# Performance work log

Hardware: AMD Instinct MI355X
Metric: run time of the kernel (lower is better)

Reference implementation:

```python
import jax, jax.numpy as jnp
import numpy as np

B, T, F, H, O = 16384, 128, 9, 128, 12


def setup_inputs() -> dict:
    key = jax.random.key(0)
    ks = jax.random.split(key, 14)
    s = 1.0 / np.sqrt(H)
    u = lambda k, shp: jax.random.uniform(k, shp, jnp.float32, -s, s)
    return {
        "x": jax.random.normal(ks[0], (B, T, F), jnp.float32),
        "W_in": u(ks[1], (H, F)), "b_in": u(ks[2], (H,)),
        "Wih0": u(ks[3], (4 * H, H)), "Whh0": u(ks[4], (4 * H, H)),
        "bih0": u(ks[5], (4 * H,)), "bhh0": u(ks[6], (4 * H,)),
        "Wih1": u(ks[7], (4 * H, H)), "Whh1": u(ks[8], (4 * H, H)),
        "bih1": u(ks[9], (4 * H,)), "bhh1": u(ks[10], (4 * H,)),
        "W_out": u(ks[11], (O, H)), "b_out": u(ks[12], (O,)),
    }


def _cell(h, c, xp, Wih, Whh, bih, bhh):
    # PyTorch LSTM gate order: i, f, g, o
    g = xp @ Wih.T + bih + h @ Whh.T + bhh  # [B, 4H]
    i, f, gg, o = jnp.split(g, 4, axis=-1)
    c = jax.nn.sigmoid(f) * c + jax.nn.sigmoid(i) * jnp.tanh(gg)
    h = jax.nn.sigmoid(o) * jnp.tanh(c)
    return h, c


def reference(x, W_in, b_in, Wih0, Whh0, bih0, bhh0, Wih1, Whh1, bih1, bhh1, W_out, b_out):
    # input projection, all timesteps at once: [B, T, H] -> scan over time
    xp = jnp.einsum('btf,hf->tbh', x, W_in) + b_in
    b = x.shape[0]
    zeros = jnp.zeros((b, H), x.dtype)
    carry0 = (zeros, zeros, zeros, zeros)  # h0, c0, h1, c1

    def step(carry, xt):
        h0, c0, h1, c1 = carry
        h0, c0 = _cell(h0, c0, xt, Wih0, Whh0, bih0, bhh0)
        h1, c1 = _cell(h1, c1, h0, Wih1, Whh1, bih1, bhh1)
        return (h0, c0, h1, c1), None

    (h0, c0, h1, c1), _ = jax.lax.scan(step, carry0, xp)
    # torch forward returns only the LAST step's output: out(h1) with softmax over dim=1
    return jax.nn.softmax(h1 @ W_out.T + b_out, axis=1)
```

## Files before the change

kernel.cpp:

```cpp
#include <hip/hip_runtime.h>
#include <stdint.h>
#include <stddef.h>

#define T_STEPS 128
#define F_IN 9
#define HID 128
#define OUT_N 12
#define XROW (T_STEPS * F_IN)

typedef __attribute__((ext_vector_type(8))) short bf16x8;
typedef __attribute__((ext_vector_type(4))) float f32x4;

#define MFMA16(a, b, c) __builtin_amdgcn_mfma_f32_16x16x32_bf16((a), (b), (c), 0, 0, 0)

__device__ __forceinline__ short f2bf(float f) {
  union { float f; uint32_t u; } v; v.f = f;
  return (short)((v.u + 0x7fffu + ((v.u >> 16) & 1u)) >> 16);
}
__device__ __forceinline__ float frcp(float x) { return __builtin_amdgcn_rcpf(x); }
__device__ __forceinline__ float fexp2(float x) { return __builtin_amdgcn_exp2f(x); }
__device__ __forceinline__ float tanh_f(float x) {
  return 1.0f - 2.0f * frcp(1.0f + fexp2(2.8853900817779268f * x));
}

__global__ void prep_w0x(const float* __restrict__ W_in, const float* __restrict__ b_in,
                         const float* __restrict__ Wih0, const float* __restrict__ bih0,
                         const float* __restrict__ bhh0, const float* __restrict__ bih1,
                         const float* __restrict__ bhh1,
                         short* __restrict__ w0xf, float* __restrict__ b0x, float* __restrict__ b1) {
  int tid = threadIdx.x;
  int nt = tid >> 4, hl = tid & 15;
  int w = nt >> 2, g = nt & 3;
  int n = g * 128 + w * 16 + hl;
  float wacc[F_IN];
#pragma unroll
  for (int f = 0; f < F_IN; ++f) wacc[f] = 0.f;
  float bacc = 0.f;
  for (int h = 0; h < HID; ++h) {
    float wv = Wih0[n * HID + h];
    bacc += wv * b_in[h];
#pragma unroll
    for (int f = 0; f < F_IN; ++f) wacc[f] += wv * W_in[h * F_IN + f];
  }
  b0x[n] = bacc + bih0[n] + bhh0[n];
  b1[n] = bih1[n] + bhh1[n];
#pragma unroll
  for (int k = 0; k < 32; ++k) {
    int quad = k >> 3, j = k & 7;
    w0xf[((w * 4 + g) * 64 + quad * 16 + hl) * 8 + j] = (k < F_IN) ? f2bf(wacc[k]) : (short)0;
  }
}

__global__ void prep_wrec(const float* __restrict__ Whh0, const float* __restrict__ Wih1,
                          const float* __restrict__ Whh1,
                          short* __restrict__ whh0f, short* __restrict__ w1f) {
  int gt = blockIdx.x * blockDim.x + threadIdx.x;
  if (gt < 2048) {
    int kt = gt >> 9, rr = gt & 511;
    int nt = rr >> 4, hl = rr & 15;
    int w = nt >> 2, g = nt & 3;
    int n = g * 128 + w * 16 + hl;
#pragma unroll
    for (int k = 0; k < 32; ++k) {
      int quad = k >> 3, j = k & 7;
      whh0f[((w * 16 + kt * 4 + g) * 64 + quad * 16 + hl) * 8 + j] =
          f2bf(Whh0[n * HID + kt * 32 + k]);
    }
  } else {
    int g2 = gt - 2048;
    int kt = g2 >> 9, rr = g2 & 511;
    int nt = rr >> 4, hl = rr & 15;
    int w = nt >> 2, g = nt & 3;
    int n = g * 128 + w * 16 + hl;
#pragma unroll
    for (int k = 0; k < 32; ++k) {
      int quad = k >> 3, j = k & 7;
      int kg = kt * 32 + k;
      float v = (kg < HID) ? Wih1[n * HID + kg] : Whh1[n * HID + kg - HID];
      w1f[((w * 32 + kt * 4 + g) * 64 + quad * 16 + hl) * 8 + j] = f2bf(v);
    }
  }
}

__global__ void __launch_bounds__(512) __attribute__((amdgpu_waves_per_eu(2)))
lstm_main(const float* __restrict__ x, const short* __restrict__ w0xf,
          const short* __restrict__ whh0f, const short* __restrict__ w1f,
          const float* __restrict__ b0x, const float* __restrict__ b1,
          const float* __restrict__ Wout, const float* __restrict__ bout,
          float* __restrict__ out) {
  __shared__ short sh[32768];
  __shared__ float h1fp[64 * HID];
  __shared__ float lg[64 * OUT_N];

  const int tid = threadIdx.x;
  const int w = tid >> 6, lane = tid & 63;
  const int quad = lane >> 4, c = lane & 15;
  const int rowbase = blockIdx.x * 64;

  {
    int* si = (int*)sh;
    for (int i = tid; i < 16384; i += 512) si[i] = 0;
  }

  short* h0_cur = sh;
  short* h0_prv = sh + 8192;
  short* h1_cur = sh + 16384;
  short* h1_prv = sh + 24576;

  const short* wp0 = w0xf + (w * 4) * 512 + lane * 8;
  const short* wph = whh0f + (w * 16) * 512 + lane * 8;
  const short* wp1 = w1f + (w * 32) * 512 + lane * 8;

  float sb0[4], sb1[4];
#pragma unroll
  for (int g = 0; g < 4; ++g) {
    int n = g * 128 + w * 16 + c;
    float bv0 = b0x[n], bv1 = b1[n];
    sb0[g] = (g == 2) ? 2.8853900817779268f * bv0 : -1.4426950408889634f * bv0;
    sb1[g] = (g == 2) ? 2.8853900817779268f * bv1 : -1.4426950408889634f * bv1;
  }

  const int kt_w = w >> 1;
  const int klocal = ((w & 1) << 4) + c;
  const int quadA = klocal >> 3;
  const int jA = klocal & 7;
  const int wr_off = (kt_w * 64 + quadA * 16 + quad * 4) * 8 + jA;

  float c0[16], c1[16];
#pragma unroll
  for (int i = 0; i < 16; ++i) { c0[i] = 0.f; c1[i] = 0.f; }

  const f32x4 z4 = {0.f, 0.f, 0.f, 0.f};

  __syncthreads();

  {
    bf16x8 xf[4];
#pragma unroll
    for (int mt = 0; mt < 4; ++mt) {
      bf16x8 v;
#pragma unroll
      for (int j = 0; j < 8; ++j) v[j] = 0;
      if (quad == 0) {
        const float* xp = x + (size_t)(rowbase + mt * 16 + c) * XROW;
#pragma unroll
        for (int j = 0; j < 8; ++j) v[j] = f2bf(xp[j]);
      } else if (quad == 1) {
        v[0] = f2bf(x[(size_t)(rowbase + mt * 16 + c) * XROW + 8]);
      }
      xf[mt] = v;
    }
    f32x4 acc[4][4];
    {
      bf16x8 b0_ = *(const bf16x8*)(wp0);
      bf16x8 b1_ = *(const bf16x8*)(wp0 + 512);
      bf16x8 b2_ = *(const bf16x8*)(wp0 + 1024);
      bf16x8 b3_ = *(const bf16x8*)(wp0 + 1536);
#pragma unroll
      for (int mt = 0; mt < 4; ++mt) {
        acc[mt][0] = MFMA16(xf[mt], b0_, z4);
        acc[mt][1] = MFMA16(xf[mt], b1_, z4);
        acc[mt][2] = MFMA16(xf[mt], b2_, z4);
        acc[mt][3] = MFMA16(xf[mt], b3_, z4);
      }
    }
#pragma unroll
    for (int mt = 0; mt < 4; ++mt)
#pragma unroll
      for (int r = 0; r < 4; ++r) {
        float gi = frcp(1.0f + fexp2(fmaf(-1.4426950408889634f, acc[mt][0][r], sb0[0])));
        float gf = frcp(1.0f + fexp2(fmaf(-1.4426950408889634f, acc[mt][1][r], sb0[1])));
        float gg = 1.0f - 2.0f * frcp(1.0f + fexp2(fmaf(2.8853900817779268f, acc[mt][2][r], sb0[2])));
        float go = frcp(1.0f + fexp2(fmaf(-1.4426950408889634f, acc[mt][3][r], sb0[3])));
        float cn = gi * gg;
        c0[mt * 4 + r] = cn;
        float hn = go * tanh_f(cn);
        h0_cur[mt * 2048 + r * 8 + wr_off] = f2bf(hn);
      }
  }
  __syncthreads();
  {
    short* tp = h0_cur; h0_cur = h0_prv; h0_prv = tp;
    tp = h1_cur; h1_cur = h1_prv; h1_prv = tp;
  }

#pragma clang loop unroll(disable)
  for (int t = 1; t < T_STEPS; ++t) {
    bf16x8 xf[4];
#pragma unroll
    for (int mt = 0; mt < 4; ++mt) {
      bf16x8 v;
#pragma unroll
      for (int j = 0; j < 8; ++j) v[j] = 0;
      if (quad == 0) {
        const float* xp = x + (size_t)(rowbase + mt * 16 + c) * XROW + t * F_IN;
#pragma unroll
        for (int j = 0; j < 8; ++j) v[j] = f2bf(xp[j]);
      } else if (quad == 1) {
        v[0] = f2bf(x[(size_t)(rowbase + mt * 16 + c) * XROW + t * F_IN + 8]);
      }
      xf[mt] = v;
    }
    {
      f32x4 acc[4][4];
      {
        const short* wb = wp1;
        bf16x8 b0_ = *(const bf16x8*)(wb);
        bf16x8 b1_ = *(const bf16x8*)(wb + 512);
        bf16x8 b2_ = *(const bf16x8*)(wb + 1024);
        bf16x8 b3_ = *(const bf16x8*)(wb + 1536);
#pragma unroll
        for (int mt = 0; mt < 4; ++mt) {
          bf16x8 af = *(const bf16x8*)(h0_prv + ((mt * 4 + 0) * 64 + lane) * 8);
          acc[mt][0] = MFMA16(af, b0_, z4);
          acc[mt][1] = MFMA16(af, b1_, z4);
          acc[mt][2] = MFMA16(af, b2_, z4);
          acc[mt][3] = MFMA16(af, b3_, z4);
        }
      }
#pragma clang loop unroll_count(3)
      for (int kt = 1; kt < 4; ++kt) {
        const short* wb = wp1 + kt * 2048;
        bf16x8 b0_ = *(const bf16x8*)(wb);
        bf16x8 b1_ = *(const bf16x8*)(wb + 512);
        bf16x8 b2_ = *(const bf16x8*)(wb + 1024);
        bf16x8 b3_ = *(const bf16x8*)(wb + 1536);
#pragma unroll
        for (int mt = 0; mt < 4; ++mt) {
          bf16x8 af = *(const bf16x8*)(h0_prv + ((mt * 4 + kt) * 64 + lane) * 8);
          acc[mt][0] = MFMA16(af, b0_, acc[mt][0]);
          acc[mt][1] = MFMA16(af, b1_, acc[mt][1]);
          acc[mt][2] = MFMA16(af, b2_, acc[mt][2]);
          acc[mt][3] = MFMA16(af, b3_, acc[mt][3]);
        }
      }
#pragma clang loop unroll_count(2)
      for (int kt = 0; kt < 4; ++kt) {
        const short* wb = wp1 + (kt + 4) * 2048;
        bf16x8 b0_ = *(const bf16x8*)(wb);
        bf16x8 b1_ = *(const bf16x8*)(wb + 512);
        bf16x8 b2_ = *(const bf16x8*)(wb + 1024);
        bf16x8 b3_ = *(const bf16x8*)(wb + 1536);
#pragma unroll
        for (int mt = 0; mt < 4; ++mt) {
          bf16x8 af = *(const bf16x8*)(h1_prv + ((mt * 4 + kt) * 64 + lane) * 8);
          acc[mt][0] = MFMA16(af, b0_, acc[mt][0]);
          acc[mt][1] = MFMA16(af, b1_, acc[mt][1]);
          acc[mt][2] = MFMA16(af, b2_, acc[mt][2]);
          acc[mt][3] = MFMA16(af, b3_, acc[mt][3]);
        }
      }
#pragma unroll
      for (int mt = 0; mt < 4; ++mt)
#pragma unroll
        for (int r = 0; r < 4; ++r) {
          float gi = frcp(1.0f + fexp2(fmaf(-1.4426950408889634f, acc[mt][0][r], sb1[0])));
          float gf = frcp(1.0f + fexp2(fmaf(-1.4426950408889634f, acc[mt][1][r], sb1[1])));
          float gg = 1.0f - 2.0f * frcp(1.0f + fexp2(fmaf(2.8853900817779268f, acc[mt][2][r], sb1[2])));
          float go = frcp(1.0f + fexp2(fmaf(-1.4426950408889634f, acc[mt][3][r], sb1[3])));
          float cn = gf * c1[mt * 4 + r] + gi * gg;
          c1[mt * 4 + r] = cn;
          float hn = go * tanh_f(cn);
          h1_cur[mt * 2048 + r * 8 + wr_off] = f2bf(hn);
        }
    }
    {
      f32x4 acc[4][4];
      {
        bf16x8 b0_ = *(const bf16x8*)(wp0);
        bf16x8 b1_ = *(const bf16x8*)(wp0 + 512);
        bf16x8 b2_ = *(const bf16x8*)(wp0 + 1024);
        bf16x8 b3_ = *(const bf16x8*)(wp0 + 1536);
#pragma unroll
        for (int mt = 0; mt < 4; ++mt) {
          acc[mt][0] = MFMA16(xf[mt], b0_, z4);
          acc[mt][1] = MFMA16(xf[mt], b1_, z4);
          acc[mt][2] = MFMA16(xf[mt], b2_, z4);
          acc[mt][3] = MFMA16(xf[mt], b3_, z4);
        }
      }
#pragma clang loop unroll_count(2)
      for (int kt = 0; kt < 4; ++kt) {
        const short* wb = wph + kt * 2048;
        bf16x8 b0_ = *(const bf16x8*)(wb);
        bf16x8 b1_ = *(const bf16x8*)(wb + 512);
        bf16x8 b2_ = *(const bf16x8*)(wb + 1024);
        bf16x8 b3_ = *(const bf16x8*)(wb + 1536);
#pragma unroll
        for (int mt = 0; mt < 4; ++mt) {
          bf16x8 af = *(const bf16x8*)(h0_prv + ((mt * 4 + kt) * 64 + lane) * 8);
          acc[mt][0] = MFMA16(af, b0_, acc[mt][0]);
          acc[mt][1] = MFMA16(af, b1_, acc[mt][1]);
          acc[mt][2] = MFMA16(af, b2_, acc[mt][2]);
          acc[mt][3] = MFMA16(af, b3_, acc[mt][3]);
        }
      }
#pragma unroll
      for (int mt = 0; mt < 4; ++mt)
#pragma unroll
        for (int r = 0; r < 4; ++r) {
          float gi = frcp(1.0f + fexp2(fmaf(-1.4426950408889634f, acc[mt][0][r], sb0[0])));
          float gf = frcp(1.0f + fexp2(fmaf(-1.4426950408889634f, acc[mt][1][r], sb0[1])));
          float gg = 1.0f - 2.0f * frcp(1.0f + fexp2(fmaf(2.8853900817779268f, acc[mt][2][r], sb0[2])));
          float go = frcp(1.0f + fexp2(fmaf(-1.4426950408889634f, acc[mt][3][r], sb0[3])));
          float cn = gf * c0[mt * 4 + r] + gi * gg;
          c0[mt * 4 + r] = cn;
          float hn = go * tanh_f(cn);
          h0_cur[mt * 2048 + r * 8 + wr_off] = f2bf(hn);
        }
    }
    __syncthreads();
    short* tp = h0_cur; h0_cur = h0_prv; h0_prv = tp;
    tp = h1_cur; h1_cur = h1_prv; h1_prv = tp;
  }

  {
    f32x4 acc[4][4];
    {
      const short* wb = wp1;
      bf16x8 b0_ = *(const bf16x8*)(wb);
      bf16x8 b1_ = *(const bf16x8*)(wb + 512);
      bf16x8 b2_ = *(const bf16x8*)(wb + 1024);
      bf16x8 b3_ = *(const bf16x8*)(wb + 1536);
#pragma unroll
      for (int mt = 0; mt < 4; ++mt) {
        bf16x8 af = *(const bf16x8*)(h0_prv + ((mt * 4 + 0) * 64 + lane) * 8);
        acc[mt][0] = MFMA16(af, b0_, z4);
        acc[mt][1] = MFMA16(af, b1_, z4);
        acc[mt][2] = MFMA16(af, b2_, z4);
        acc[mt][3] = MFMA16(af, b3_, z4);
      }
    }
#pragma unroll
    for (int kt = 1; kt < 4; ++kt) {
      const short* wb = wp1 + kt * 2048;
      bf16x8 b0_ = *(const bf16x8*)(wb);
      bf16x8 b1_ = *(const bf16x8*)(wb + 512);
      bf16x8 b2_ = *(const bf16x8*)(wb + 1024);
      bf16x8 b3_ = *(const bf16x8*)(wb + 1536);
#pragma unroll
      for (int mt = 0; mt < 4; ++mt) {
        bf16x8 af = *(const bf16x8*)(h0_prv + ((mt * 4 + kt) * 64 + lane) * 8);
        acc[mt][0] = MFMA16(af, b0_, acc[mt][0]);
        acc[mt][1] = MFMA16(af, b1_, acc[mt][1]);
        acc[mt][2] = MFMA16(af, b2_, acc[mt][2]);
        acc[mt][3] = MFMA16(af, b3_, acc[mt][3]);
      }
    }
#pragma unroll
    for (int kt = 0; kt < 4; ++kt) {
      const short* wb = wp1 + (kt + 4) * 2048;
      bf16x8 b0_ = *(const bf16x8*)(wb);
      bf16x8 b1_ = *(const bf16x8*)(wb + 512);
      bf16x8 b2_ = *(const bf16x8*)(wb + 1024);
      bf16x8 b3_ = *(const bf16x8*)(wb + 1536);
#pragma unroll
      for (int mt = 0; mt < 4; ++mt) {
        bf16x8 af = *(const bf16x8*)(h1_prv + ((mt * 4 + kt) * 64 + lane) * 8);
        acc[mt][0] = MFMA16(af, b0_, acc[mt][0]);
        acc[mt][1] = MFMA16(af, b1_, acc[mt][1]);
        acc[mt][2] = MFMA16(af, b2_, acc[mt][2]);
        acc[mt][3] = MFMA16(af, b3_, acc[mt][3]);
      }
    }
#pragma unroll
    for (int mt = 0; mt < 4; ++mt)
#pragma unroll
      for (int r = 0; r < 4; ++r) {
        float gi = frcp(1.0f + fexp2(fmaf(-1.4426950408889634f, acc[mt][0][r], sb1[0])));
        float gf = frcp(1.0f + fexp2(fmaf(-1.4426950408889634f, acc[mt][1][r], sb1[1])));
        float gg = 1.0f - 2.0f * frcp(1.0f + fexp2(fmaf(2.8853900817779268f, acc[mt][2][r], sb1[2])));
        float go = frcp(1.0f + fexp2(fmaf(-1.4426950408889634f, acc[mt][3][r], sb1[3])));
        float cn = gf * c1[mt * 4 + r] + gi * gg;
        float hn = go * tanh_f(cn);
        h1fp[(mt * 16 + quad * 4 + r) * HID + w * 16 + c] = hn;
      }
  }
  __syncthreads();

  {
    int row = tid >> 3, og = tid & 7;
    for (int oc = og; oc < OUT_N; oc += 8) {
      float s = bout[oc];
      const float* wo = Wout + oc * HID;
      const float* hr = h1fp + row * HID;
#pragma unroll 8
      for (int k = 0; k < HID; ++k) s += hr[k] * wo[k];
      lg[row * OUT_N + oc] = s;
    }
  }
  __syncthreads();
  if (tid < 64) {
    int row = tid;
    float m = lg[row * OUT_N];
#pragma unroll
    for (int oc = 1; oc < OUT_N; ++oc) m = fmaxf(m, lg[row * OUT_N + oc]);
    float e[OUT_N];
    float s = 0.f;
#pragma unroll
    for (int oc = 0; oc < OUT_N; ++oc) {
      e[oc] = __expf(lg[row * OUT_N + oc] - m);
      s += e[oc];
    }
    float inv = 1.0f / s;
    float* orow = out + (size_t)(rowbase + row) * OUT_N;
#pragma unroll
    for (int oc = 0; oc < OUT_N; ++oc) orow[oc] = e[oc] * inv;
  }
}

extern "C" void kernel_launch(void* const* d_in, const int* in_sizes, int n_in,
                              void* d_out, int out_size, void* d_ws, size_t ws_size,
                              hipStream_t stream) {
  const float* x    = (const float*)d_in[0];
  const float* W_in = (const float*)d_in[1];
  const float* b_in = (const float*)d_in[2];
  const float* Wih0 = (const float*)d_in[3];
  const float* Whh0 = (const float*)d_in[4];
  const float* bih0 = (const float*)d_in[5];
  const float* bhh0 = (const float*)d_in[6];
  const float* Wih1 = (const float*)d_in[7];
  const float* Whh1 = (const float*)d_in[8];
  const float* bih1 = (const float*)d_in[9];
  const float* bhh1 = (const float*)d_in[10];
  const float* Wout = (const float*)d_in[11];
  const float* bout = (const float*)d_in[12];
  float* out = (float*)d_out;

  short* w0xf  = (short*)d_ws;
  short* whh0f = w0xf + 16384;
  short* w1f   = whh0f + 65536;
  float* b0x   = (float*)(w1f + 131072);
  float* b1    = b0x + 512;

  prep_w0x<<<1, 512, 0, stream>>>(W_in, b_in, Wih0, bih0, bhh0, bih1, bhh1, w0xf, b0x, b1);
  prep_wrec<<<12, 512, 0, stream>>>(Whh0, Wih1, Whh1, whh0f, w1f);
  lstm_main<<<256, 512, 0, stream>>>(x, w0xf, whh0f, w1f, b0x, b1, Wout, bout, out);
}
```

Baseline: 1.341 ms.

## Split each block's M-tiles across two waves per gate column, doubling block size

```diff
diff --git a/kernel.cpp b/kernel.cpp
--- a/kernel.cpp
+++ b/kernel.cpp
@@ -82,7 +82,7 @@
   }
 }
 
-__global__ void __launch_bounds__(512) __attribute__((amdgpu_waves_per_eu(2)))
+__global__ void __launch_bounds__(1024) __attribute__((amdgpu_waves_per_eu(4)))
 lstm_main(const float* __restrict__ x, const short* __restrict__ w0xf,
           const short* __restrict__ whh0f, const short* __restrict__ w1f,
           const float* __restrict__ b0x, const float* __restrict__ b1,
@@ -93,13 +93,16 @@
   __shared__ float lg[64 * OUT_N];
 
   const int tid = threadIdx.x;
-  const int w = tid >> 6, lane = tid & 63;
+  const int wid = tid >> 6, lane = tid & 63;
+  const int w = wid >> 1;
+  const int mh = wid & 1;
+  const int mtb = mh * 2;
   const int quad = lane >> 4, c = lane & 15;
   const int rowbase = blockIdx.x * 64;
 
   {
     int* si = (int*)sh;
-    for (int i = tid; i < 16384; i += 512) si[i] = 0;
+    for (int i = tid; i < 16384; i += 1024) si[i] = 0;
   }
 
   short* h0_cur = sh;
@@ -126,18 +129,19 @@
   const int jA = klocal & 7;
   const int wr_off = (kt_w * 64 + quadA * 16 + quad * 4) * 8 + jA;
 
-  float c0[16], c1[16];
-#pragma unroll
-  for (int i = 0; i < 16; ++i) { c0[i] = 0.f; c1[i] = 0.f; }
+  float c0[8], c1[8];
+#pragma unroll
+  for (int i = 0; i < 8; ++i) { c0[i] = 0.f; c1[i] = 0.f; }
 
   const f32x4 z4 = {0.f, 0.f, 0.f, 0.f};
 
   __syncthreads();
 
   {
-    bf16x8 xf[4];
-#pragma unroll
-    for (int mt = 0; mt < 4; ++mt) {
+    bf16x8 xf[2];
+#pragma unroll
+    for (int m = 0; m < 2; ++m) {
+      int mt = mtb + m;
       bf16x8 v;
 #pragma unroll
       for (int j = 0; j < 8; ++j) v[j] = 0;
@@ -148,34 +152,34 @@
       } else if (quad == 1) {
         v[0] = f2bf(x[(size_t)(rowbase + mt * 16 + c) * XROW + 8]);
       }
-      xf[mt] = v;
-    }
-    f32x4 acc[4][4];
+      xf[m] = v;
+    }
+    f32x4 acc[2][4];
     {
       bf16x8 b0_ = *(const bf16x8*)(wp0);
       bf16x8 b1_ = *(const bf16x8*)(wp0 + 512);
       bf16x8 b2_ = *(const bf16x8*)(wp0 + 1024);
       bf16x8 b3_ = *(const bf16x8*)(wp0 + 1536);
 #pragma unroll
-      for (int mt = 0; mt < 4; ++mt) {
-        acc[mt][0] = MFMA16(xf[mt], b0_, z4);
-        acc[mt][1] = MFMA16(xf[mt], b1_, z4);
-        acc[mt][2] = MFMA16(xf[mt], b2_, z4);
-        acc[mt][3] = MFMA16(xf[mt], b3_, z4);
-      }
-    }
-#pragma unroll
-    for (int mt = 0; mt < 4; ++mt)
+      for (int m = 0; m < 2; ++m) {
+        acc[m][0] = MFMA16(xf[m], b0_, z4);
+        acc[m][1] = MFMA16(xf[m], b1_, z4);
+        acc[m][2] = MFMA16(xf[m], b2_, z4);
+        acc[m][3] = MFMA16(xf[m], b3_, z4);
+      }
+    }
+#pragma unroll
+    for (int m = 0; m < 2; ++m)
 #pragma unroll
       for (int r = 0; r < 4; ++r) {
-        float gi = frcp(1.0f + fexp2(fmaf(-1.4426950408889634f, acc[mt][0][r], sb0[0])));
-        float gf = frcp(1.0f + fexp2(fmaf(-1.4426950408889634f, acc[mt][1][r], sb0[1])));
-        float gg = 1.0f - 2.0f * frcp(1.0f + fexp2(fmaf(2.8853900817779268f, acc[mt][2][r], sb0[2])));
-        float go = frcp(1.0f + fexp2(fmaf(-1.4426950408889634f, acc[mt][3][r], sb0[3])));
+        float gi = frcp(1.0f + fexp2(fmaf(-1.4426950408889634f, acc[m][0][r], sb0[0])));
+        float gf = frcp(1.0f + fexp2(fmaf(-1.4426950408889634f, acc[m][1][r], sb0[1])));
+        float gg = 1.0f - 2.0f * frcp(1.0f + fexp2(fmaf(2.8853900817779268f, acc[m][2][r], sb0[2])));
+        float go = frcp(1.0f + fexp2(fmaf(-1.4426950408889634f, acc[m][3][r], sb0[3])));
         float cn = gi * gg;
-        c0[mt * 4 + r] = cn;
+        c0[m * 4 + r] = cn;
         float hn = go * tanh_f(cn);
-        h0_cur[mt * 2048 + r * 8 + wr_off] = f2bf(hn);
+        h0_cur[(mtb + m) * 2048 + r * 8 + wr_off] = f2bf(hn);
       }
   }
   __syncthreads();
@@ -186,9 +190,10 @@
 
 #pragma clang loop unroll(disable)
   for (int t = 1; t < T_STEPS; ++t) {
-    bf16x8 xf[4];
-#pragma unroll
-    for (int mt = 0; mt < 4; ++mt) {
+    bf16x8 xf[2];
+#pragma unroll
+    for (int m = 0; m < 2; ++m) {
+      int mt = mtb + m;
       bf16x8 v;
 #pragma unroll
       for (int j = 0; j < 8; ++j) v[j] = 0;
@@ -199,10 +204,10 @@
       } else if (quad == 1) {
         v[0] = f2bf(x[(size_t)(rowbase + mt * 16 + c) * XROW + t * F_IN + 8]);
       }
-      xf[mt] = v;
+      xf[m] = v;
     }
     {
-      f32x4 acc[4][4];
+      f32x4 acc[2][4];
       {
         const short* wb = wp1;
         bf16x8 b0_ = *(const bf16x8*)(wb);
@@ -210,12 +215,12 @@
         bf16x8 b2_ = *(const bf16x8*)(wb + 1024);
         bf16x8 b3_ = *(const bf16x8*)(wb + 1536);
 #pragma unroll
-        for (int mt = 0; mt < 4; ++mt) {
-          bf16x8 af = *(const bf16x8*)(h0_prv + ((mt * 4 + 0) * 64 + lane) * 8);
-          acc[mt][0] = MFMA16(af, b0_, z4);
-          acc[mt][1] = MFMA16(af, b1_, z4);
-          acc[mt][2] = MFMA16(af, b2_, z4);
-          acc[mt][3] = MFMA16(af, b3_, z4);
+        for (int m = 0; m < 2; ++m) {
+          bf16x8 af = *(const bf16x8*)(h0_prv + (((mtb + m) * 4 + 0) * 64 + lane) * 8);
+          acc[m][0] = MFMA16(af, b0_, z4);
+          acc[m][1] = MFMA16(af, b1_, z4);
+          acc[m][2] = MFMA16(af, b2_, z4);
+          acc[m][3] = MFMA16(af, b3_, z4);
         }
       }
 #pragma clang loop unroll_count(3)
@@ -226,12 +231,12 @@
         bf16x8 b2_ = *(const bf16x8*)(wb + 1024);
         bf16x8 b3_ = *(const bf16x8*)(wb + 1536);
 #pragma unroll
-        for (int mt = 0; mt < 4; ++mt) {
-          bf16x8 af = *(const bf16x8*)(h0_prv + ((mt * 4 + kt) * 64 + lane) * 8);
-          acc[mt][0] = MFMA16(af, b0_, acc[mt][0]);
-          acc[mt][1] = MFMA16(af, b1_, acc[mt][1]);
-          acc[mt][2] = MFMA16(af, b2_, acc[mt][2]);
-          acc[mt][3] = MFMA16(af, b3_, acc[mt][3]);
+        for (int m = 0; m < 2; ++m) {
+          bf16x8 af = *(const bf16x8*)(h0_prv + (((mtb + m) * 4 + kt) * 64 + lane) * 8);
+          acc[m][0] = MFMA16(af, b0_, acc[m][0]);
+          acc[m][1] = MFMA16(af, b1_, acc[m][1]);
+          acc[m][2] = MFMA16(af, b2_, acc[m][2]);
+          acc[m][3] = MFMA16(af, b3_, acc[m][3]);
         }
       }
 #pragma clang loop unroll_count(2)
@@ -242,41 +247,41 @@
         bf16x8 b2_ = *(const bf16x8*)(wb + 1024);
         bf16x8 b3_ = *(const bf16x8*)(wb + 1536);
 #pragma unroll
-        for (int mt = 0; mt < 4; ++mt) {
-          bf16x8 af = *(const bf16x8*)(h1_prv + ((mt * 4 + kt) * 64 + lane) * 8);
-          acc[mt][0] = MFMA16(af, b0_, acc[mt][0]);
-          acc[mt][1] = MFMA16(af, b1_, acc[mt][1]);
-          acc[mt][2] = MFMA16(af, b2_, acc[mt][2]);
-          acc[mt][3] = MFMA16(af, b3_, acc[mt][3]);
-        }
-      }
-#pragma unroll
-      for (int mt = 0; mt < 4; ++mt)
+        for (int m = 0; m < 2; ++m) {
+          bf16x8 af = *(const bf16x8*)(h1_prv + (((mtb + m) * 4 + kt) * 64 + lane) * 8);
+          acc[m][0] = MFMA16(af, b0_, acc[m][0]);
+          acc[m][1] = MFMA16(af, b1_, acc[m][1]);
+          acc[m][2] = MFMA16(af, b2_, acc[m][2]);
+          acc[m][3] = MFMA16(af, b3_, acc[m][3]);
+        }
+      }
+#pragma unroll
+      for (int m = 0; m < 2; ++m)
 #pragma unroll
         for (int r = 0; r < 4; ++r) {
-          float gi = frcp(1.0f + fexp2(fmaf(-1.4426950408889634f, acc[mt][0][r], sb1[0])));
-          float gf = frcp(1.0f + fexp2(fmaf(-1.4426950408889634f, acc[mt][1][r], sb1[1])));
-          float gg = 1.0f - 2.0f * frcp(1.0f + fexp2(fmaf(2.8853900817779268f, acc[mt][2][r], sb1[2])));
-          float go = frcp(1.0f + fexp2(fmaf(-1.4426950408889634f, acc[mt][3][r], sb1[3])));
-          float cn = gf * c1[mt * 4 + r] + gi * gg;
-          c1[mt * 4 + r] = cn;
+          float gi = frcp(1.0f + fexp2(fmaf(-1.4426950408889634f, acc[m][0][r], sb1[0])));
+          float gf = frcp(1.0f + fexp2(fmaf(-1.4426950408889634f, acc[m][1][r], sb1[1])));
+          float gg = 1.0f - 2.0f * frcp(1.0f + fexp2(fmaf(2.8853900817779268f, acc[m][2][r], sb1[2])));
+          float go = frcp(1.0f + fexp2(fmaf(-1.4426950408889634f, acc[m][3][r], sb1[3])));
+          float cn = gf * c1[m * 4 + r] + gi * gg;
+          c1[m * 4 + r] = cn;
           float hn = go * tanh_f(cn);
-          h1_cur[mt * 2048 + r * 8 + wr_off] = f2bf(hn);
+          h1_cur[(mtb + m) * 2048 + r * 8 + wr_off] = f2bf(hn);
         }
     }
     {
-      f32x4 acc[4][4];
+      f32x4 acc[2][4];
       {
         bf16x8 b0_ = *(const bf16x8*)(wp0);
         bf16x8 b1_ = *(const bf16x8*)(wp0 + 512);
         bf16x8 b2_ = *(const bf16x8*)(wp0 + 1024);
         bf16x8 b3_ = *(const bf16x8*)(wp0 + 1536);
 #pragma unroll
-        for (int mt = 0; mt < 4; ++mt) {
-          acc[mt][0] = MFMA16(xf[mt], b0_, z4);
-          acc[mt][1] = MFMA16(xf[mt], b1_, z4);
-          acc[mt][2] = MFMA16(xf[mt], b2_, z4);
-          acc[mt][3] = MFMA16(xf[mt], b3_, z4);
+        for (int m = 0; m < 2; ++m) {
+          acc[m][0] = MFMA16(xf[m], b0_, z4);
+          acc[m][1] = MFMA16(xf[m], b1_, z4);
+          acc[m][2] = MFMA16(xf[m], b2_, z4);
+          acc[m][3] = MFMA16(xf[m], b3_, z4);
         }
       }
 #pragma clang loop unroll_count(2)
@@ -287,26 +292,26 @@
         bf16x8 b2_ = *(const bf16x8*)(wb + 1024);
         bf16x8 b3_ = *(const bf16x8*)(wb + 1536);
 #pragma unroll
-        for (int mt = 0; mt < 4; ++mt) {
-          bf16x8 af = *(const bf16x8*)(h0_prv + ((mt * 4 + kt) * 64 + lane) * 8);
-          acc[mt][0] = MFMA16(af, b0_, acc[mt][0]);
-          acc[mt][1] = MFMA16(af, b1_, acc[mt][1]);
-          acc[mt][2] = MFMA16(af, b2_, acc[mt][2]);
-          acc[mt][3] = MFMA16(af, b3_, acc[mt][3]);
-        }
-      }
-#pragma unroll
-      for (int mt = 0; mt < 4; ++mt)
+        for (int m = 0; m < 2; ++m) {
+          bf16x8 af = *(const bf16x8*)(h0_prv + (((mtb + m) * 4 + kt) * 64 + lane) * 8);
+          acc[m][0] = MFMA16(af, b0_, acc[m][0]);
+          acc[m][1] = MFMA16(af, b1_, acc[m][1]);
+          acc[m][2] = MFMA16(af, b2_, acc[m][2]);
+          acc[m][3] = MFMA16(af, b3_, acc[m][3]);
+        }
+      }
+#pragma unroll
+      for (int m = 0; m < 2; ++m)
 #pragma unroll
         for (int r = 0; r < 4; ++r) {
-          float gi = frcp(1.0f + fexp2(fmaf(-1.4426950408889634f, acc[mt][0][r], sb0[0])));
-          float gf = frcp(1.0f + fexp2(fmaf(-1.4426950408889634f, acc[mt][1][r], sb0[1])));
-          float gg = 1.0f - 2.0f * frcp(1.0f + fexp2(fmaf(2.8853900817779268f, acc[mt][2][r], sb0[2])));
-          float go = frcp(1.0f + fexp2(fmaf(-1.4426950408889634f, acc[mt][3][r], sb0[3])));
-          float cn = gf * c0[mt * 4 + r] + gi * gg;
-          c0[mt * 4 + r] = cn;
+          float gi = frcp(1.0f + fexp2(fmaf(-1.4426950408889634f, acc[m][0][r], sb0[0])));
+          float gf = frcp(1.0f + fexp2(fmaf(-1.4426950408889634f, acc[m][1][r], sb0[1])));
+          float gg = 1.0f - 2.0f * frcp(1.0f + fexp2(fmaf(2.8853900817779268f, acc[m][2][r], sb0[2])));
+          float go = frcp(1.0f + fexp2(fmaf(-1.4426950408889634f, acc[m][3][r], sb0[3])));
+          float cn = gf * c0[m * 4 + r] + gi * gg;
+          c0[m * 4 + r] = cn;
           float hn = go * tanh_f(cn);
-          h0_cur[mt * 2048 + r * 8 + wr_off] = f2bf(hn);
+          h0_cur[(mtb + m) * 2048 + r * 8 + wr_off] = f2bf(hn);
         }
     }
     __syncthreads();
@@ -315,7 +320,7 @@
   }
 
   {
-    f32x4 acc[4][4];
+    f32x4 acc[2][4];
     {
       const short* wb = wp1;
       bf16x8 b0_ = *(const bf16x8*)(wb);
@@ -323,12 +328,12 @@
       bf16x8 b2_ = *(const bf16x8*)(wb + 1024);
       bf16x8 b3_ = *(const bf16x8*)(wb + 1536);
 #pragma unroll
-      for (int mt = 0; mt < 4; ++mt) {
-        bf16x8 af = *(const bf16x8*)(h0_prv + ((mt * 4 + 0) * 64 + lane) * 8);
-        acc[mt][0] = MFMA16(af, b0_, z4);
-        acc[mt][1] = MFMA16(af, b1_, z4);
-        acc[mt][2] = MFMA16(af, b2_, z4);
-        acc[mt][3] = MFMA16(af, b3_, z4);
+      for (int m = 0; m < 2; ++m) {
+        bf16x8 af = *(const bf16x8*)(h0_prv + (((mtb + m) * 4 + 0) * 64 + lane) * 8);
+        acc[m][0] = MFMA16(af, b0_, z4);
+        acc[m][1] = MFMA16(af, b1_, z4);
+        acc[m][2] = MFMA16(af, b2_, z4);
+        acc[m][3] = MFMA16(af, b3_, z4);
       }
     }
 #pragma unroll
@@ -339,12 +344,12 @@
       bf16x8 b2_ = *(const bf16x8*)(wb + 1024);
       bf16x8 b3_ = *(const bf16x8*)(wb + 1536);
 #pragma unroll
-      for (int mt = 0; mt < 4; ++mt) {
-        bf16x8 af = *(const bf16x8*)(h0_prv + ((mt * 4 + kt) * 64 + lane) * 8);
-        acc[mt][0] = MFMA16(af, b0_, acc[mt][0]);
-        acc[mt][1] = MFMA16(af, b1_, acc[mt][1]);
-        acc[mt][2] = MFMA16(af, b2_, acc[mt][2]);
-        acc[mt][3] = MFMA16(af, b3_, acc[mt][3]);
+      for (int m = 0; m < 2; ++m) {
+        bf16x8 af = *(const bf16x8*)(h0_prv + (((mtb + m) * 4 + kt) * 64 + lane) * 8);
+        acc[m][0] = MFMA16(af, b0_, acc[m][0]);
+        acc[m][1] = MFMA16(af, b1_, acc[m][1]);
+        acc[m][2] = MFMA16(af, b2_, acc[m][2]);
+        acc[m][3] = MFMA16(af, b3_, acc[m][3]);
       }
     }
 #pragma unroll
@@ -355,32 +360,32 @@
       bf16x8 b2_ = *(const bf16x8*)(wb + 1024);
       bf16x8 b3_ = *(const bf16x8*)(wb + 1536);
 #pragma unroll
-      for (int mt = 0; mt < 4; ++mt) {
-        bf16x8 af = *(const bf16x8*)(h1_prv + ((mt * 4 + kt) * 64 + lane) * 8);
-        acc[mt][0] = MFMA16(af, b0_, acc[mt][0]);
-        acc[mt][1] = MFMA16(af, b1_, acc[mt][1]);
-        acc[mt][2] = MFMA16(af, b2_, acc[mt][2]);
-        acc[mt][3] = MFMA16(af, b3_, acc[mt][3]);
-      }
-    }
-#pragma unroll
-    for (int mt = 0; mt < 4; ++mt)
+      for (int m = 0; m < 2; ++m) {
+        bf16x8 af = *(const bf16x8*)(h1_prv + (((mtb + m) * 4 + kt) * 64 + lane) * 8);
+        acc[m][0] = MFMA16(af, b0_, acc[m][0]);
+        acc[m][1] = MFMA16(af, b1_, acc[m][1]);
+        acc[m][2] = MFMA16(af, b2_, acc[m][2]);
+        acc[m][3] = MFMA16(af, b3_, acc[m][3]);
+      }
+    }
+#pragma unroll
+    for (int m = 0; m < 2; ++m)
 #pragma unroll
       for (int r = 0; r < 4; ++r) {
-        float gi = frcp(1.0f + fexp2(fmaf(-1.4426950408889634f, acc[mt][0][r], sb1[0])));
-        float gf = frcp(1.0f + fexp2(fmaf(-1.4426950408889634f, acc[mt][1][r], sb1[1])));
-        float gg = 1.0f - 2.0f * frcp(1.0f + fexp2(fmaf(2.8853900817779268f, acc[mt][2][r], sb1[2])));
-        float go = frcp(1.0f + fexp2(fmaf(-1.4426950408889634f, acc[mt][3][r], sb1[3])));
-        float cn = gf * c1[mt * 4 + r] + gi * gg;
+        float gi = frcp(1.0f + fexp2(fmaf(-1.4426950408889634f, acc[m][0][r], sb1[0])));
+        float gf = frcp(1.0f + fexp2(fmaf(-1.4426950408889634f, acc[m][1][r], sb1[1])));
+        float gg = 1.0f - 2.0f * frcp(1.0f + fexp2(fmaf(2.8853900817779268f, acc[m][2][r], sb1[2])));
+        float go = frcp(1.0f + fexp2(fmaf(-1.4426950408889634f, acc[m][3][r], sb1[3])));
+        float cn = gf * c1[m * 4 + r] + gi * gg;
         float hn = go * tanh_f(cn);
-        h1fp[(mt * 16 + quad * 4 + r) * HID + w * 16 + c] = hn;
+        h1fp[((mtb + m) * 16 + quad * 4 + r) * HID + w * 16 + c] = hn;
       }
   }
   __syncthreads();
 
   {
-    int row = tid >> 3, og = tid & 7;
-    for (int oc = og; oc < OUT_N; oc += 8) {
+    int row = tid >> 4, og = tid & 15;
+    for (int oc = og; oc < OUT_N; oc += 16) {
       float s = bout[oc];
       const float* wo = Wout + oc * HID;
       const float* hr = h1fp + row * HID;
@@ -435,5 +440,5 @@
 
   prep_w0x<<<1, 512, 0, stream>>>(W_in, b_in, Wih0, bih0, bhh0, bih1, bhh1, w0xf, b0x, b1);
   prep_wrec<<<12, 512, 0, stream>>>(Whh0, Wih1, Whh1, whh0f, w1f);
-  lstm_main<<<256, 512, 0, stream>>>(x, w0xf, whh0f, w1f, b0x, b1, Wout, bout, out);
-}
+  lstm_main<<<256, 1024, 0, stream>>>(x, w0xf, whh0f, w1f, b0x, b1, Wout, bout, out);
+}
```

After: 2.005 ms. 49.5% more time.
